# Performance work log

Hardware: AMD Instinct MI355X
Metric: run time of the kernel (lower is better)

## Reference

```python
import jax, jax.numpy as jnp
import numpy as np

N_NODES = 50000
N_REL = 8
N_EDGES = 100000
IN_SIZE = 128
OUT_SIZE = 128


def setup_inputs() -> dict:
    key = jax.random.key(0)
    k1, k2, k3, k4, k5 = jax.random.split(key, 5)
    inp = jax.random.normal(k1, (N_NODES, IN_SIZE), dtype=jnp.float32)
    src = jax.random.randint(k2, (N_REL, N_EDGES), 0, N_NODES, dtype=jnp.int32)
    dst = jax.random.randint(k3, (N_REL, N_EDGES), 0, N_NODES, dtype=jnp.int32)
    vals = jax.random.uniform(k4, (N_REL, N_EDGES), dtype=jnp.float32)
    weights = jax.random.normal(k5, (N_REL, IN_SIZE, OUT_SIZE), dtype=jnp.float32) * (1.0 / np.sqrt(IN_SIZE))
    return {"inp": inp, "src": src, "dst": dst, "vals": vals, "weights": weights}


def reference(inp, src, dst, vals, weights):
    # Per-relation sparse adj @ inp:  agg[r] = A_r @ inp, A_r given as COO edges.
    n_nodes = inp.shape[0]

    def rel_agg(s, d, v):
        msgs = v[:, None] * inp[s]                      # [E, in]
        return jax.ops.segment_sum(msgs, d, num_segments=n_nodes)  # [N, in]

    agg = jax.vmap(rel_agg)(src, dst, vals)             # [R, N, in]
    # concat along features then block-stacked weight matmul == per-relation
    # matmul summed over relations: out = sum_r agg[r] @ W[r]
    out = jnp.einsum('rni,rio->no', agg, weights)       # [N, out]
    return out
```

## Files before the change

### kernel.cpp

```cpp
#include <hip/hip_runtime.h>


constexpr int IN  = 128;
constexpr int OUT = 128;
constexpr int LDK = 136;
constexpr int NPB = 64;
constexpr int NGRP = 512;
constexpr int MAXE = 2048;
constexpr int NXCD = 8;
constexpr int CPAD = 16;

typedef __attribute__((ext_vector_type(8))) short bf16x8;
typedef __attribute__((ext_vector_type(4))) float f32x4;

__device__ inline unsigned short f2bf(float f) {
    unsigned int u = __float_as_uint(f);
    u += 0x7fffu + ((u >> 16) & 1u);
    return (unsigned short)(u >> 16);
}
__device__ inline float bflo(unsigned int u) { return __uint_as_float(u << 16); }
__device__ inline float bfhi(unsigned int u) { return __uint_as_float(u & 0xffff0000u); }

__global__ __launch_bounds__(256) void conv_inp_kernel(
    const float* __restrict__ x, unsigned short* __restrict__ y, int n8)
{
    const int i = blockIdx.x * 256 + threadIdx.x;
    if (i >= n8) return;
    const float4 a = ((const float4*)x)[i * 2];
    const float4 b = ((const float4*)x)[i * 2 + 1];
    uint4 o;
    o.x = (unsigned)f2bf(a.x) | ((unsigned)f2bf(a.y) << 16);
    o.y = (unsigned)f2bf(a.z) | ((unsigned)f2bf(a.w) << 16);
    o.z = (unsigned)f2bf(b.x) | ((unsigned)f2bf(b.y) << 16);
    o.w = (unsigned)f2bf(b.z) | ((unsigned)f2bf(b.w) << 16);
    ((uint4*)y)[i] = o;
}

__global__ __launch_bounds__(256) void conv_w_kernel(
    const float* __restrict__ w, unsigned short* __restrict__ wt, int total)
{
    const int t = blockIdx.x * 256 + threadIdx.x;
    if (t >= total) return;
    const int r = t >> 14, rem = t & 16383;
    const int n = rem >> 7, k = rem & 127;
    wt[t] = f2bf(w[(r << 14) + (k << 7) + n]);
}

__global__ __launch_bounds__(256) void prep_kernel(
    const float* __restrict__ x, unsigned short* __restrict__ y, int n8, int nbI,
    const float* __restrict__ w, unsigned short* __restrict__ wtb, int wtot, int nbW,
    const int* __restrict__ src, const int* __restrict__ dst,
    const float* __restrict__ vals, int* __restrict__ bin_cnt,
    int2* __restrict__ binned, int4* __restrict__ spill,
    int* __restrict__ spill_cnt,
    int n_edges, int n_nodes, int nbins, int cap, int spill_max, int fill_gx)
{
    const int bid = blockIdx.x;
    const int tid = threadIdx.x;
    if (bid < nbI) {
        const int i = bid * 256 + tid;
        if (i >= n8) return;
        const float4 a = ((const float4*)x)[i * 2];
        const float4 b = ((const float4*)x)[i * 2 + 1];
        uint4 o;
        o.x = (unsigned)f2bf(a.x) | ((unsigned)f2bf(a.y) << 16);
        o.y = (unsigned)f2bf(a.z) | ((unsigned)f2bf(a.w) << 16);
        o.z = (unsigned)f2bf(b.x) | ((unsigned)f2bf(b.y) << 16);
        o.w = (unsigned)f2bf(b.z) | ((unsigned)f2bf(b.w) << 16);
        ((uint4*)y)[i] = o;
        return;
    }
    if (bid < nbI + nbW) {
        const int t = (bid - nbI) * 256 + tid;
        if (t >= wtot) return;
        const int r = t >> 14, rem = t & 16383;
        const int n = rem >> 7, k = rem & 127;
        wtb[t] = f2bf(w[(r << 14) + (k << 7) + n]);
        return;
    }
    int xcd;
    asm volatile("s_getreg_b32 %0, hwreg(HW_REG_XCC_ID)" : "=s"(xcd));
    xcd &= (NXCD - 1);
    const int idx = bid - nbI - nbW;
    const int rel = idx / fill_gx;
    const int e = (idx - rel * fill_gx) * 256 + tid;
    if (e >= n_edges) return;
    const size_t g = (size_t)rel * n_edges + e;
    const int d = dst[g];
    const int s = src[g];
    const int bin = d >> 6;
    const int packed = (rel << 25) | ((d & 63) << 19) | s;
    const int cell = xcd * nbins + bin;
    const int pos = atomicAdd(&bin_cnt[cell * CPAD], 1);
    if (pos < cap) {
        binned[(size_t)cell * cap + pos] =
            make_int2(packed, __float_as_int(vals[g]));
    } else {
        const int sp = atomicAdd(spill_cnt, 1);
        if (sp < spill_max)
            spill[sp] = make_int4(d, (rel << 19) | s, __float_as_int(vals[g]), 0);
    }
}

__global__ __launch_bounds__(256) void bin_gather_gemm(
    const unsigned short* __restrict__ inpb,
    const unsigned short* __restrict__ wt,
    const int2* __restrict__ binned, const int* __restrict__ bin_cnt,
    float* __restrict__ out, int n_nodes, int nbins, int cap, int n_rel)
{
    __shared__ int2 sorted[MAXE];
    __shared__ unsigned short A[64 * LDK];
    __shared__ int lcnt[NGRP], loff[NGRP], lcur[NGRP];
    __shared__ int cellcnt[NXCD];

    const int bin = blockIdx.x;
    const int tid = threadIdx.x;

    for (int i = tid; i < NGRP; i += 256) lcnt[i] = 0;
    if (tid < NXCD) {
        int c = bin_cnt[(tid * nbins + bin) * CPAD];
        cellcnt[tid] = c > cap ? cap : c;
    }
    __syncthreads();

    for (int xc = 0; xc < NXCD; ++xc) {
        const int cnt = cellcnt[xc];
        const int2* __restrict__ b = binned + (size_t)(xc * nbins + bin) * cap;
        for (int i = tid; i < cnt; i += 256)
            atomicAdd(&lcnt[(b[i].x >> 19) & (NGRP - 1)], 1);
    }
    __syncthreads();

    if (tid < 64) {
        const int base = tid * 8;
        int v[8]; int s = 0;
        #pragma unroll
        for (int i = 0; i < 8; ++i) { v[i] = s; s += lcnt[base + i]; }
        int incl = s;
        #pragma unroll
        for (int off = 1; off < 64; off <<= 1) {
            int t = __shfl_up(incl, off, 64);
            if (tid >= off) incl += t;
        }
        const int excl = incl - s;
        #pragma unroll
        for (int i = 0; i < 8; ++i) loff[base + i] = excl + v[i];
    }
    for (int i = tid; i < NGRP; i += 256) lcur[i] = 0;
    __syncthreads();

    for (int xc = 0; xc < NXCD; ++xc) {
        const int cnt = cellcnt[xc];
        const int2* __restrict__ b = binned + (size_t)(xc * nbins + bin) * cap;
        for (int i = tid; i < cnt; i += 256) {
            const int2 e = b[i];
            const int g = (e.x >> 19) & (NGRP - 1);
            const int pos = atomicAdd(&lcur[g], 1);
            sorted[loff[g] + pos] = e;
        }
    }
    __syncthreads();

    const int wave = tid >> 6, lane = tid & 63;
    const int m = lane & 15, q = lane >> 4;
    const int hw = tid >> 5, hlane = tid & 31;

    f32x4 acc[4][2];
    #pragma unroll
    for (int mt = 0; mt < 4; ++mt) {
        acc[mt][0] = (f32x4){0.f, 0.f, 0.f, 0.f};
        acc[mt][1] = (f32x4){0.f, 0.f, 0.f, 0.f};
    }

    for (int r = 0; r < n_rel; ++r) {
        #pragma unroll
        for (int k = 0; k < 8; ++k) {
            const int ln = hw * 8 + k;
            const int g = r * 64 + ln;
            const int base = loff[g], cnt = lcnt[g];
            float4 a4 = make_float4(0.f, 0.f, 0.f, 0.f);
            int j = 0;
            for (; j + 4 <= cnt; j += 4) {
                const int2 r0 = sorted[base + j],     r1 = sorted[base + j + 1];
                const int2 r2 = sorted[base + j + 2], r3 = sorted[base + j + 3];
                const uint2 h0 = ((const uint2*)(inpb + (size_t)(r0.x & 0x7ffff) * IN))[hlane];
                const uint2 h1 = ((const uint2*)(inpb + (size_t)(r1.x & 0x7ffff) * IN))[hlane];
                const uint2 h2 = ((const uint2*)(inpb + (size_t)(r2.x & 0x7ffff) * IN))[hlane];
                const uint2 h3 = ((const uint2*)(inpb + (size_t)(r3.x & 0x7ffff) * IN))[hlane];
                const float v0 = __int_as_float(r0.y), v1 = __int_as_float(r1.y);
                const float v2 = __int_as_float(r2.y), v3 = __int_as_float(r3.y);
                a4.x += v0*bflo(h0.x) + v1*bflo(h1.x) + v2*bflo(h2.x) + v3*bflo(h3.x);
                a4.y += v0*bfhi(h0.x) + v1*bfhi(h1.x) + v2*bfhi(h2.x) + v3*bfhi(h3.x);
                a4.z += v0*bflo(h0.y) + v1*bflo(h1.y) + v2*bflo(h2.y) + v3*bflo(h3.y);
                a4.w += v0*bfhi(h0.y) + v1*bfhi(h1.y) + v2*bfhi(h2.y) + v3*bfhi(h3.y);
            }
            for (; j < cnt; ++j) {
                const int2 r0 = sorted[base + j];
                const float v = __int_as_float(r0.y);
                const uint2 hv = ((const uint2*)(inpb + (size_t)(r0.x & 0x7ffff) * IN))[hlane];
                a4.x += v * bflo(hv.x); a4.y += v * bfhi(hv.x);
                a4.z += v * bflo(hv.y); a4.w += v * bfhi(hv.y);
            }
            uint2 o;
            o.x = (unsigned)f2bf(a4.x) | ((unsigned)f2bf(a4.y) << 16);
            o.y = (unsigned)f2bf(a4.z) | ((unsigned)f2bf(a4.w) << 16);
            *(uint2*)&A[ln * LDK + hlane * 4] = o;
        }
        __syncthreads();

        const unsigned short* wtr = wt + ((size_t)r * OUT + wave * 32) * IN;
        bf16x8 bfrag[2][4];
        #pragma unroll
        for (int nt = 0; nt < 2; ++nt)
            #pragma unroll
            for (int ks = 0; ks < 4; ++ks)
                bfrag[nt][ks] = *(const bf16x8*)(
                    wtr + (size_t)(nt * 16 + m) * IN + ks * 32 + q * 8);

        #pragma unroll
        for (int ks = 0; ks < 4; ++ks) {
            bf16x8 a[4];
            #pragma unroll
            for (int mt = 0; mt < 4; ++mt)
                a[mt] = *(const bf16x8*)&A[(mt * 16 + m) * LDK + ks * 32 + q * 8];
            #pragma unroll
            for (int mt = 0; mt < 4; ++mt) {
                acc[mt][0] = __builtin_amdgcn_mfma_f32_16x16x32_bf16(
                    a[mt], bfrag[0][ks], acc[mt][0], 0, 0, 0);
                acc[mt][1] = __builtin_amdgcn_mfma_f32_16x16x32_bf16(
                    a[mt], bfrag[1][ks], acc[mt][1], 0, 0, 0);
            }
        }
        __syncthreads();
    }

    const int row0 = bin * NPB;
    #pragma unroll
    for (int mt = 0; mt < 4; ++mt) {
        #pragma unroll
        for (int rg = 0; rg < 4; ++rg) {
            const int row = row0 + mt * 16 + q * 4 + rg;
            if (row < n_nodes) {
                float* op = out + (size_t)row * OUT + wave * 32 + m;
                op[0]  = acc[mt][0][rg];
                op[16] = acc[mt][1][rg];
            }
        }
    }
}

__global__ __launch_bounds__(256) void spill_w_kernel(
    const unsigned short* __restrict__ inpb,
    const unsigned short* __restrict__ wt,
    const int4* __restrict__ spill, const int* __restrict__ spill_cnt,
    float* __restrict__ out, int spill_max)
{
    int n = *spill_cnt;
    if (n > spill_max) n = spill_max;
    const int w = (blockIdx.x * 256 + threadIdx.x) >> 6;
    const int lane = threadIdx.x & 63;
    const int nw = gridDim.x * 4;
    for (int i = w; i < n; i += nw) {
        const int4 s = spill[i];
        const int d = s.x;
        const int rel = s.y >> 19, srcrow = s.y & 0x7ffff;
        const float v = __int_as_float(s.z);
        const unsigned short* irow = inpb + (size_t)srcrow * IN;
        #pragma unroll
        for (int cc = 0; cc < 2; ++cc) {
            const int col = lane * 2 + cc;
            const unsigned short* wrow = wt + ((size_t)rel * OUT + col) * IN;
            float acc = 0.f;
            for (int k8 = 0; k8 < IN; k8 += 8) {
                const uint4 iw = *(const uint4*)(irow + k8);
                const uint4 ww = *(const uint4*)(wrow + k8);
                acc += bflo(iw.x)*bflo(ww.x) + bfhi(iw.x)*bfhi(ww.x)
                     + bflo(iw.y)*bflo(ww.y) + bfhi(iw.y)*bfhi(ww.y)
                     + bflo(iw.z)*bflo(ww.z) + bfhi(iw.z)*bfhi(ww.z)
                     + bflo(iw.w)*bflo(ww.w) + bfhi(iw.w)*bfhi(ww.w);
            }
            __hip_atomic_fetch_add(out + (size_t)d * OUT + col, v * acc,
                                   __ATOMIC_RELAXED, __HIP_MEMORY_SCOPE_AGENT);
        }
    }
}

__global__ __launch_bounds__(256) void mfma_gemm(
    const unsigned short* __restrict__ inpb,
    const unsigned short* __restrict__ wt,
    unsigned short* __restrict__ h, int rel_base, int n_nodes)
{
    __shared__ unsigned short As[128 * LDK];

    const int rel = rel_base + blockIdx.y;
    const int row0 = blockIdx.x * 128;
    const int tid = threadIdx.x;
    const int wave = tid >> 6, lane = tid & 63;
    const int m = lane & 15, q = lane >> 4;

    {
        const int r = tid >> 1;
        const int half = (tid & 1) * 64;
        const int grow = row0 + r;
        const uint4* gp = (const uint4*)(inpb + (size_t)grow * IN + half);
        uint4* lp = (uint4*)&As[r * LDK + half];
        #pragma unroll
        for (int i = 0; i < 8; ++i) {
            uint4 v = make_uint4(0u, 0u, 0u, 0u);
            if (grow < n_nodes) v = gp[i];
            lp[i] = v;
        }
    }

    bf16x8 bfrag[2][4];
    {
        const unsigned short* wtr = wt + ((size_t)rel * OUT + wave * 32) * IN;
        #pragma unroll
        for (int nt = 0; nt < 2; ++nt)
            #pragma unroll
            for (int ks = 0; ks < 4; ++ks)
                bfrag[nt][ks] = *(const bf16x8*)(
                    wtr + (size_t)(nt * 16 + m) * IN + ks * 32 + q * 8);
    }

    __syncthreads();

    f32x4 acc[8][2];
    #pragma unroll
    for (int mt = 0; mt < 8; ++mt)
        #pragma unroll
        for (int nt = 0; nt < 2; ++nt)
            acc[mt][nt] = (f32x4){0.f, 0.f, 0.f, 0.f};

    #pragma unroll
    for (int ks = 0; ks < 4; ++ks) {
        bf16x8 a[8];
        #pragma unroll
        for (int mt = 0; mt < 8; ++mt)
            a[mt] = *(const bf16x8*)&As[(mt * 16 + m) * LDK + ks * 32 + q * 8];
        #pragma unroll
        for (int mt = 0; mt < 8; ++mt) {
            acc[mt][0] = __builtin_amdgcn_mfma_f32_16x16x32_bf16(
                a[mt], bfrag[0][ks], acc[mt][0], 0, 0, 0);
            acc[mt][1] = __builtin_amdgcn_mfma_f32_16x16x32_bf16(
                a[mt], bfrag[1][ks], acc[mt][1], 0, 0, 0);
        }
    }

    unsigned short* hrel = h + (size_t)blockIdx.y * n_nodes * OUT;
    #pragma unroll
    for (int mt = 0; mt < 8; ++mt) {
        #pragma unroll
        for (int rg = 0; rg < 4; ++rg) {
            const int row = row0 + mt * 16 + q * 4 + rg;
            if (row < n_nodes) {
                unsigned short* hp = hrel + (size_t)row * OUT + wave * 32 + m;
                hp[0]  = f2bf(acc[mt][0][rg]);
                hp[16] = f2bf(acc[mt][1][rg]);
            }
        }
    }
}

__global__ __launch_bounds__(256) void fill_kernel(
    const int* __restrict__ src, const int* __restrict__ dst,
    const float* __restrict__ vals, int* __restrict__ counts,
    int2* __restrict__ bucket, int4* __restrict__ spill,
    int* __restrict__ spill_cnt, int n_edges, int n_nodes,
    int cap, int spill_max)
{
    const int e = blockIdx.x * 256 + threadIdx.x;
    if (e >= n_edges) return;
    const size_t g = (size_t)blockIdx.y * n_edges + e;
    const int d = dst[g];
    const int enc = blockIdx.y * n_nodes + src[g];
    const int pos = atomicAdd(&counts[d], 1);
    if (pos < cap) {
        bucket[(size_t)d * cap + pos] = make_int2(enc, __float_as_int(vals[g]));
    } else {
        const int sp = atomicAdd(spill_cnt, 1);
        if (sp < spill_max)
            spill[sp] = make_int4(d, enc, __float_as_int(vals[g]), 0);
    }
}

__global__ __launch_bounds__(256) void gather_kernel(
    const unsigned short* __restrict__ h, const int2* __restrict__ bucket,
    const int* __restrict__ counts, float* __restrict__ out,
    int n_nodes, int cap, int accum)
{
    const int node = blockIdx.x * 8 + (threadIdx.x >> 5);
    const int lane = threadIdx.x & 31;
    if (node >= n_nodes) return;
    int cnt = counts[node];
    if (cnt > cap) cnt = cap;
    const int2* __restrict__ b = bucket + (size_t)node * cap;
    float4* __restrict__ op = (float4*)(out + (size_t)node * OUT);

    float4 acc = accum ? op[lane] : make_float4(0.f, 0.f, 0.f, 0.f);
    int j = 0;
    for (; j + 4 <= cnt; j += 4) {
        const int2 r0 = b[j], r1 = b[j + 1], r2 = b[j + 2], r3 = b[j + 3];
        const uint2 h0 = ((const uint2*)(h + (size_t)r0.x * OUT))[lane];
        const uint2 h1 = ((const uint2*)(h + (size_t)r1.x * OUT))[lane];
        const uint2 h2 = ((const uint2*)(h + (size_t)r2.x * OUT))[lane];
        const uint2 h3 = ((const uint2*)(h + (size_t)r3.x * OUT))[lane];
        const float v0 = __int_as_float(r0.y), v1 = __int_as_float(r1.y);
        const float v2 = __int_as_float(r2.y), v3 = __int_as_float(r3.y);
        acc.x += v0*bflo(h0.x) + v1*bflo(h1.x) + v2*bflo(h2.x) + v3*bflo(h3.x);
        acc.y += v0*bfhi(h0.x) + v1*bfhi(h1.x) + v2*bfhi(h2.x) + v3*bfhi(h3.x);
        acc.z += v0*bflo(h0.y) + v1*bflo(h1.y) + v2*bflo(h2.y) + v3*bflo(h3.y);
        acc.w += v0*bfhi(h0.y) + v1*bfhi(h1.y) + v2*bfhi(h2.y) + v3*bfhi(h3.y);
    }
    for (; j < cnt; ++j) {
        const int2 r0 = b[j];
        const float v = __int_as_float(r0.y);
        const uint2 hv = ((const uint2*)(h + (size_t)r0.x * OUT))[lane];
        acc.x += v * bflo(hv.x); acc.y += v * bfhi(hv.x);
        acc.z += v * bflo(hv.y); acc.w += v * bfhi(hv.y);
    }
    op[lane] = acc;
}

__global__ __launch_bounds__(256) void spill_kernel(
    const unsigned short* __restrict__ h, const int4* __restrict__ spill,
    const int* __restrict__ spill_cnt, float* __restrict__ out, int spill_max)
{
    int n = *spill_cnt;
    if (n > spill_max) n = spill_max;
    const int w = (blockIdx.x * 256 + threadIdx.x) >> 6;
    const int lane = threadIdx.x & 63;
    const int nw = gridDim.x * 4;
    for (int i = w; i < n; i += nw) {
        const int4 s = spill[i];
        const float v = __int_as_float(s.z);
        const unsigned int u = ((const unsigned int*)(h + (size_t)s.y * OUT))[lane];
        float* __restrict__ orow = out + (size_t)s.x * OUT;
        __hip_atomic_fetch_add(orow + lane * 2,     v * bflo(u),
                               __ATOMIC_RELAXED, __HIP_MEMORY_SCOPE_AGENT);
        __hip_atomic_fetch_add(orow + lane * 2 + 1, v * bfhi(u),
                               __ATOMIC_RELAXED, __HIP_MEMORY_SCOPE_AGENT);
    }
}

__global__ __launch_bounds__(256) void scatter_kernel(
    const unsigned short* __restrict__ h, const int* __restrict__ src,
    const int* __restrict__ dst, const float* __restrict__ vals,
    float* __restrict__ out, int n_edges)
{
    const int e = blockIdx.x * 8 + (threadIdx.x >> 5);
    if (e >= n_edges) return;
    const int lane = threadIdx.x & 31;
    const int s = src[e];
    const int d = dst[e];
    const float v = vals[e];
    const unsigned int* __restrict__ hrow =
        (const unsigned int*)(h + (size_t)s * OUT);
    float* __restrict__ orow = out + (size_t)d * OUT;
    #pragma unroll
    for (int kk = 0; kk < 2; ++kk) {
        const int jj = lane + kk * 32;
        const unsigned int u = hrow[jj];
        __hip_atomic_fetch_add(orow + jj * 2,     v * bflo(u),
                               __ATOMIC_RELAXED, __HIP_MEMORY_SCOPE_AGENT);
        __hip_atomic_fetch_add(orow + jj * 2 + 1, v * bfhi(u),
                               __ATOMIC_RELAXED, __HIP_MEMORY_SCOPE_AGENT);
    }
}

extern "C" void kernel_launch(void* const* d_in, const int* in_sizes, int n_in,
                              void* d_out, int out_size, void* d_ws, size_t ws_size,
                              hipStream_t stream) {
    const float* inp     = (const float*)d_in[0];
    const int*   src     = (const int*)  d_in[1];
    const int*   dst     = (const int*)  d_in[2];
    const float* vals    = (const float*)d_in[3];
    const float* weights = (const float*)d_in[4];
    float* out = (float*)d_out;

    const int n_nodes = in_sizes[0] / IN;
    const int n_rel   = in_sizes[4] / (IN * OUT);
    const int n_edges = in_sizes[1] / n_rel;

    auto align_up = [](size_t x) { return (x + 255) & ~(size_t)255; };
    const int SPILL_MAX = 65536;
    const size_t sz_inpb   = align_up((size_t)n_nodes * IN * 2);
    const size_t sz_wt     = align_up((size_t)n_rel * IN * OUT * 2);
    const size_t sz_spill  = align_up((size_t)SPILL_MAX * 16);

    const int conv_n8 = n_nodes * IN / 8;
    const int wt_tot  = n_rel * IN * OUT;
    const int gemm_gx = (n_nodes + 127) / 128;
    const int gath_gx = (n_nodes + 7) / 8;
    const int fill_gx = (n_edges + 255) / 256;
    const int nbins   = (n_nodes + NPB - 1) / NPB;

    if (n_rel <= 8 && n_nodes < (1 << 19)) {
        const size_t sz_bcnt = align_up(((size_t)NXCD * nbins * CPAD + CPAD) * 4);
        int cap = 0;
        const int caps[] = {256, 192};
        for (int c : caps) {
            const size_t sz_binned = align_up((size_t)NXCD * nbins * c * 8);
            if (sz_inpb + sz_wt + sz_bcnt + sz_spill + sz_binned <= ws_size) {
                cap = c; break;
            }
        }
        if (cap > 0) {
            const size_t sz_binned = align_up((size_t)NXCD * nbins * cap * 8);
            char* p = (char*)d_ws;
            unsigned short* inpb = (unsigned short*)p;  p += sz_inpb;
            unsigned short* wtb  = (unsigned short*)p;  p += sz_wt;
            int*   bin_cnt = (int*)p;   p += sz_bcnt;
            int4*  spill   = (int4*)p;  p += sz_spill;
            int2*  binned  = (int2*)p;  p += sz_binned;
            int*   spill_cnt = bin_cnt + (size_t)NXCD * nbins * CPAD;

            const int nbI = (conv_n8 + 255) / 256;
            const int nbW = (wt_tot + 255) / 256;
            const int nF  = fill_gx * n_rel;

            hipMemsetAsync(bin_cnt, 0,
                           ((size_t)NXCD * nbins * CPAD + CPAD) * 4, stream);
            prep_kernel<<<nbI + nbW + nF, 256, 0, stream>>>(
                inp, inpb, conv_n8, nbI, weights, wtb, wt_tot, nbW,
                src, dst, vals, bin_cnt, binned, spill, spill_cnt,
                n_edges, n_nodes, nbins, cap, SPILL_MAX, fill_gx);
            bin_gather_gemm<<<nbins, 256, 0, stream>>>(
                inpb, wtb, binned, bin_cnt, out, n_nodes, nbins, cap, n_rel);
            spill_w_kernel<<<128, 256, 0, stream>>>(
                inpb, wtb, spill, spill_cnt, out, SPILL_MAX);
            return;
        }
    }

    const size_t sz_counts = align_up((size_t)(n_nodes + 1) * 4);
    const size_t fixed = sz_inpb + sz_wt + sz_counts + sz_spill;

    {
        const size_t sz_h = (size_t)n_rel * n_nodes * OUT * 2;
        int cap = 0;
        const int caps[] = {64, 48, 32, 24, 20};
        for (int c : caps) {
            if (fixed + sz_h + align_up((size_t)n_nodes * c * 8) <= ws_size) {
                cap = c; break;
            }
        }
        if (cap > 0) {
            char* p = (char*)d_ws;
            unsigned short* inpb = (unsigned short*)p;  p += sz_inpb;
            unsigned short* wtb  = (unsigned short*)p;  p += sz_wt;
            int*   counts = (int*)p;    p += sz_counts;
            int4*  spill  = (int4*)p;   p += sz_spill;
            unsigned short* h = (unsigned short*)p;     p += sz_h;
            int2*  bucket = (int2*)p;
            int*   spill_cnt = counts + n_nodes;

            conv_inp_kernel<<<(conv_n8 + 255) / 256, 256, 0, stream>>>(
                inp, inpb, conv_n8);
            conv_w_kernel<<<(wt_tot + 255) / 256, 256, 0, stream>>>(
                weights, wtb, wt_tot);
            hipMemsetAsync(counts, 0, (size_t)(n_nodes + 1) * 4, stream);
            dim3 fg(fill_gx, n_rel);
            fill_kernel<<<fg, 256, 0, stream>>>(src, dst, vals, counts, bucket,
                                                spill, spill_cnt, n_edges,
                                                n_nodes, cap, SPILL_MAX);
            dim3 gg(gemm_gx, n_rel);
            mfma_gemm<<<gg, 256, 0, stream>>>(inpb, wtb, h, 0, n_nodes);
            gather_kernel<<<gath_gx, 256, 0, stream>>>(h, bucket, counts, out,
                                                       n_nodes, cap, 0);
            spill_kernel<<<128, 256, 0, stream>>>(h, spill, spill_cnt, out,
                                                  SPILL_MAX);
            return;
        }
    }

    {
        char* p = (char*)d_ws;
        unsigned short* inpb = (unsigned short*)p;  p += sz_inpb;
        unsigned short* wtb  = (unsigned short*)p;  p += sz_wt;
        unsigned short* h = (unsigned short*)p;

        conv_inp_kernel<<<(conv_n8 + 255) / 256, 256, 0, stream>>>(
            inp, inpb, conv_n8);
        conv_w_kernel<<<(wt_tot + 255) / 256, 256, 0, stream>>>(
            weights, wtb, wt_tot);
        hipMemsetAsync(out, 0, (size_t)n_nodes * OUT * 4, stream);
        const int sgx = (n_edges + 7) / 8;
        for (int r = 0; r < n_rel; ++r) {
            const size_t eoff = (size_t)r * n_edges;
            dim3 gg(gemm_gx, 1);
            mfma_gemm<<<gg, 256, 0, stream>>>(inpb, wtb, h, r, n_nodes);
            scatter_kernel<<<sgx, 256, 0, stream>>>(h, src + eoff, dst + eoff,
                                                    vals + eoff, out, n_edges);
        }
    }
}
```

Before: 221.6 us.

## Bin edges per relation and aggregate via LDS float atomics instead of sorting

Edge binning cells now include the relation index, so each block reads per-relation lists directly and drops the in-block counting sort over 512 groups. Aggregation switches from a per-row serial gather to parallel edge processing that scatters into an fp32 LDS tile with atomicAdd, then converts to bf16 when loading MFMA fragments. This removes the sort passes and evens out load imbalance across destination rows, but adds many LDS atomics, a larger fp32 tile, and more bin-count cells to memset and read.

```diff
diff --git a/kernel.cpp b/kernel.cpp
--- a/kernel.cpp
+++ b/kernel.cpp
@@ -5,8 +5,8 @@
 constexpr int OUT = 128;
 constexpr int LDK = 136;
 constexpr int NPB = 64;
-constexpr int NGRP = 512;
-constexpr int MAXE = 2048;
+constexpr int LDA = 132;
+constexpr int MAXT = 512;
 constexpr int NXCD = 8;
 constexpr int CPAD = 16;
 
@@ -20,6 +20,9 @@
 }
 __device__ inline float bflo(unsigned int u) { return __uint_as_float(u << 16); }
 __device__ inline float bfhi(unsigned int u) { return __uint_as_float(u & 0xffff0000u); }
+__device__ inline unsigned int pack2bf(float a, float b) {
+    return (unsigned)f2bf(a) | ((unsigned)f2bf(b) << 16);
+}
 
 __global__ __launch_bounds__(256) void conv_inp_kernel(
     const float* __restrict__ x, unsigned short* __restrict__ y, int n8)
@@ -29,10 +32,10 @@
     const float4 a = ((const float4*)x)[i * 2];
     const float4 b = ((const float4*)x)[i * 2 + 1];
     uint4 o;
-    o.x = (unsigned)f2bf(a.x) | ((unsigned)f2bf(a.y) << 16);
-    o.y = (unsigned)f2bf(a.z) | ((unsigned)f2bf(a.w) << 16);
-    o.z = (unsigned)f2bf(b.x) | ((unsigned)f2bf(b.y) << 16);
-    o.w = (unsigned)f2bf(b.z) | ((unsigned)f2bf(b.w) << 16);
+    o.x = pack2bf(a.x, a.y);
+    o.y = pack2bf(a.z, a.w);
+    o.z = pack2bf(b.x, b.y);
+    o.w = pack2bf(b.z, b.w);
     ((uint4*)y)[i] = o;
 }
 
@@ -53,7 +56,8 @@
     const float* __restrict__ vals, int* __restrict__ bin_cnt,
     int2* __restrict__ binned, int4* __restrict__ spill,
     int* __restrict__ spill_cnt,
-    int n_edges, int n_nodes, int nbins, int cap, int spill_max, int fill_gx)
+    int n_edges, int n_nodes, int nbins, int cap, int spill_max,
+    int fill_gx, int n_rel)
 {
     const int bid = blockIdx.x;
     const int tid = threadIdx.x;
@@ -63,10 +67,10 @@
         const float4 a = ((const float4*)x)[i * 2];
         const float4 b = ((const float4*)x)[i * 2 + 1];
         uint4 o;
-        o.x = (unsigned)f2bf(a.x) | ((unsigned)f2bf(a.y) << 16);
-        o.y = (unsigned)f2bf(a.z) | ((unsigned)f2bf(a.w) << 16);
-        o.z = (unsigned)f2bf(b.x) | ((unsigned)f2bf(b.y) << 16);
-        o.w = (unsigned)f2bf(b.z) | ((unsigned)f2bf(b.w) << 16);
+        o.x = pack2bf(a.x, a.y);
+        o.y = pack2bf(a.z, a.w);
+        o.z = pack2bf(b.x, b.y);
+        o.w = pack2bf(b.z, b.w);
         ((uint4*)y)[i] = o;
         return;
     }
@@ -89,8 +93,8 @@
     const int d = dst[g];
     const int s = src[g];
     const int bin = d >> 6;
-    const int packed = (rel << 25) | ((d & 63) << 19) | s;
-    const int cell = xcd * nbins + bin;
+    const int packed = ((d & 63) << 19) | s;
+    const int cell = (xcd * n_rel + rel) * nbins + bin;
     const int pos = atomicAdd(&bin_cnt[cell * CPAD], 1);
     if (pos < cap) {
         binned[(size_t)cell * cap + pos] =
@@ -102,68 +106,39 @@
     }
 }
 
-__global__ __launch_bounds__(256) void bin_gather_gemm(
+__global__ __launch_bounds__(256, 4) void bin_gemm_kernel(
     const unsigned short* __restrict__ inpb,
     const unsigned short* __restrict__ wt,
     const int2* __restrict__ binned, const int* __restrict__ bin_cnt,
     float* __restrict__ out, int n_nodes, int nbins, int cap, int n_rel)
 {
-    __shared__ int2 sorted[MAXE];
-    __shared__ unsigned short A[64 * LDK];
-    __shared__ int lcnt[NGRP], loff[NGRP], lcur[NGRP];
-    __shared__ int cellcnt[NXCD];
+    __shared__ float A[NPB * LDA];
+    __shared__ int2 ent[MAXT];
+    __shared__ int cnt_lds[NXCD * 8];
+    __shared__ int coff[8][NXCD + 1];
 
     const int bin = blockIdx.x;
     const int tid = threadIdx.x;
 
-    for (int i = tid; i < NGRP; i += 256) lcnt[i] = 0;
-    if (tid < NXCD) {
-        int c = bin_cnt[(tid * nbins + bin) * CPAD];
-        cellcnt[tid] = c > cap ? cap : c;
+    if (tid < NXCD * n_rel) {
+        const int x = tid / n_rel, r = tid - x * n_rel;
+        int c = bin_cnt[((x * n_rel + r) * nbins + bin) * CPAD];
+        cnt_lds[x * n_rel + r] = c > cap ? cap : c;
     }
     __syncthreads();
-
-    for (int xc = 0; xc < NXCD; ++xc) {
-        const int cnt = cellcnt[xc];
-        const int2* __restrict__ b = binned + (size_t)(xc * nbins + bin) * cap;
-        for (int i = tid; i < cnt; i += 256)
-            atomicAdd(&lcnt[(b[i].x >> 19) & (NGRP - 1)], 1);
-    }
-    __syncthreads();
-
-    if (tid < 64) {
-        const int base = tid * 8;
-        int v[8]; int s = 0;
-        #pragma unroll
-        for (int i = 0; i < 8; ++i) { v[i] = s; s += lcnt[base + i]; }
-        int incl = s;
-        #pragma unroll
-        for (int off = 1; off < 64; off <<= 1) {
-            int t = __shfl_up(incl, off, 64);
-            if (tid >= off) incl += t;
-        }
-        const int excl = incl - s;
-        #pragma unroll
-        for (int i = 0; i < 8; ++i) loff[base + i] = excl + v[i];
-    }
-    for (int i = tid; i < NGRP; i += 256) lcur[i] = 0;
-    __syncthreads();
-
-    for (int xc = 0; xc < NXCD; ++xc) {
-        const int cnt = cellcnt[xc];
-        const int2* __restrict__ b = binned + (size_t)(xc * nbins + bin) * cap;
-        for (int i = tid; i < cnt; i += 256) {
-            const int2 e = b[i];
-            const int g = (e.x >> 19) & (NGRP - 1);
-            const int pos = atomicAdd(&lcur[g], 1);
-            sorted[loff[g] + pos] = e;
-        }
-    }
-    __syncthreads();
+    if (tid < n_rel) {
+        int s = 0;
+        coff[tid][0] = 0;
+        #pragma unroll
+        for (int x = 0; x < NXCD; ++x) {
+            s += cnt_lds[x * n_rel + tid];
+            coff[tid][x + 1] = s;
+        }
+    }
 
     const int wave = tid >> 6, lane = tid & 63;
     const int m = lane & 15, q = lane >> 4;
-    const int hw = tid >> 5, hlane = tid & 31;
+    const int qtr = (tid >> 4) & 3, l16 = tid & 15;
 
     f32x4 acc[4][2];
     #pragma unroll
@@ -173,38 +148,49 @@
     }
 
     for (int r = 0; r < n_rel; ++r) {
-        #pragma unroll
-        for (int k = 0; k < 8; ++k) {
-            const int ln = hw * 8 + k;
-            const int g = r * 64 + ln;
-            const int base = loff[g], cnt = lcnt[g];
-            float4 a4 = make_float4(0.f, 0.f, 0.f, 0.f);
-            int j = 0;
-            for (; j + 4 <= cnt; j += 4) {
-                const int2 r0 = sorted[base + j],     r1 = sorted[base + j + 1];
-                const int2 r2 = sorted[base + j + 2], r3 = sorted[base + j + 3];
-                const uint2 h0 = ((const uint2*)(inpb + (size_t)(r0.x & 0x7ffff) * IN))[hlane];
-                const uint2 h1 = ((const uint2*)(inpb + (size_t)(r1.x & 0x7ffff) * IN))[hlane];
-                const uint2 h2 = ((const uint2*)(inpb + (size_t)(r2.x & 0x7ffff) * IN))[hlane];
-                const uint2 h3 = ((const uint2*)(inpb + (size_t)(r3.x & 0x7ffff) * IN))[hlane];
-                const float v0 = __int_as_float(r0.y), v1 = __int_as_float(r1.y);
-                const float v2 = __int_as_float(r2.y), v3 = __int_as_float(r3.y);
-                a4.x += v0*bflo(h0.x) + v1*bflo(h1.x) + v2*bflo(h2.x) + v3*bflo(h3.x);
-                a4.y += v0*bfhi(h0.x) + v1*bfhi(h1.x) + v2*bfhi(h2.x) + v3*bfhi(h3.x);
-                a4.z += v0*bflo(h0.y) + v1*bflo(h1.y) + v2*bflo(h2.y) + v3*bflo(h3.y);
-                a4.w += v0*bfhi(h0.y) + v1*bfhi(h1.y) + v2*bfhi(h2.y) + v3*bfhi(h3.y);
-            }
-            for (; j < cnt; ++j) {
-                const int2 r0 = sorted[base + j];
-                const float v = __int_as_float(r0.y);
-                const uint2 hv = ((const uint2*)(inpb + (size_t)(r0.x & 0x7ffff) * IN))[hlane];
-                a4.x += v * bflo(hv.x); a4.y += v * bfhi(hv.x);
-                a4.z += v * bflo(hv.y); a4.w += v * bfhi(hv.y);
-            }
-            uint2 o;
-            o.x = (unsigned)f2bf(a4.x) | ((unsigned)f2bf(a4.y) << 16);
-            o.y = (unsigned)f2bf(a4.z) | ((unsigned)f2bf(a4.w) << 16);
-            *(uint2*)&A[ln * LDK + hlane * 4] = o;
+        __syncthreads();
+
+        {
+            float* zp = &A[(tid >> 2) * LDA + (tid & 3) * 32];
+            #pragma unroll
+            for (int i = 0; i < 8; ++i)
+                *(float4*)(zp + i * 4) = make_float4(0.f, 0.f, 0.f, 0.f);
+        }
+        const int T = coff[r][NXCD];
+        for (int i = tid; i < T; i += 256) {
+            int xc = 0;
+            #pragma unroll
+            for (int j = 1; j < NXCD; ++j) xc += (i >= coff[r][j]);
+            const int pos = i - coff[r][xc];
+            ent[i] = binned[(size_t)((xc * n_rel + r) * nbins + bin) * cap + pos];
+        }
+        __syncthreads();
+
+        for (int base = wave * 16 + qtr * 4; base < T; base += 64) {
+            int2 e[4];
+            #pragma unroll
+            for (int k = 0; k < 4; ++k) {
+                const int idx = base + k;
+                e[k] = (idx < T) ? ent[idx] : make_int2(0, 0);
+            }
+            uint4 rw[4];
+            #pragma unroll
+            for (int k = 0; k < 4; ++k)
+                rw[k] = ((const uint4*)(inpb +
+                         (size_t)(e[k].x & 0x7ffff) * IN))[l16];
+            #pragma unroll
+            for (int k = 0; k < 4; ++k) {
+                const float v = __int_as_float(e[k].y);
+                float* Ar = &A[((e[k].x >> 19) & 63) * LDA + l16 * 8];
+                atomicAdd(Ar + 0, v * bflo(rw[k].x));
+                atomicAdd(Ar + 1, v * bfhi(rw[k].x));
+                atomicAdd(Ar + 2, v * bflo(rw[k].y));
+                atomicAdd(Ar + 3, v * bfhi(rw[k].y));
+                atomicAdd(Ar + 4, v * bflo(rw[k].z));
+                atomicAdd(Ar + 5, v * bfhi(rw[k].z));
+                atomicAdd(Ar + 6, v * bflo(rw[k].w));
+                atomicAdd(Ar + 7, v * bfhi(rw[k].w));
+            }
         }
         __syncthreads();
 
@@ -221,8 +207,15 @@
         for (int ks = 0; ks < 4; ++ks) {
             bf16x8 a[4];
             #pragma unroll
-            for (int mt = 0; mt < 4; ++mt)
-                a[mt] = *(const bf16x8*)&A[(mt * 16 + m) * LDK + ks * 32 + q * 8];
+            for (int mt = 0; mt < 4; ++mt) {
+                const float* Ap = &A[(mt * 16 + m) * LDA + ks * 32 + q * 8];
+                const float4 lo = *(const float4*)Ap;
+                const float4 hi = *(const float4*)(Ap + 4);
+                union { uint4 u; bf16x8 v; } cv;
+                cv.u = make_uint4(pack2bf(lo.x, lo.y), pack2bf(lo.z, lo.w),
+                                  pack2bf(hi.x, hi.y), pack2bf(hi.z, hi.w));
+                a[mt] = cv.v;
+            }
             #pragma unroll
             for (int mt = 0; mt < 4; ++mt) {
                 acc[mt][0] = __builtin_amdgcn_mfma_f32_16x16x32_bf16(
@@ -231,7 +224,6 @@
                     a[mt], bfrag[1][ks], acc[mt][1], 0, 0, 0);
             }
         }
-        __syncthreads();
     }
 
     const int row0 = bin * NPB;
@@ -496,36 +488,36 @@
     const int nbins   = (n_nodes + NPB - 1) / NPB;
 
     if (n_rel <= 8 && n_nodes < (1 << 19)) {
-        const size_t sz_bcnt = align_up(((size_t)NXCD * nbins * CPAD + CPAD) * 4);
+        const size_t ncells  = (size_t)NXCD * n_rel * nbins;
+        const size_t sz_bcnt = align_up((ncells * CPAD + CPAD) * 4);
         int cap = 0;
-        const int caps[] = {256, 192};
+        const int caps[] = {64, 48, 32};
         for (int c : caps) {
-            const size_t sz_binned = align_up((size_t)NXCD * nbins * c * 8);
+            const size_t sz_binned = align_up(ncells * c * 8);
             if (sz_inpb + sz_wt + sz_bcnt + sz_spill + sz_binned <= ws_size) {
                 cap = c; break;
             }
         }
         if (cap > 0) {
-            const size_t sz_binned = align_up((size_t)NXCD * nbins * cap * 8);
+            const size_t sz_binned = align_up(ncells * cap * 8);
             char* p = (char*)d_ws;
             unsigned short* inpb = (unsigned short*)p;  p += sz_inpb;
             unsigned short* wtb  = (unsigned short*)p;  p += sz_wt;
             int*   bin_cnt = (int*)p;   p += sz_bcnt;
             int4*  spill   = (int4*)p;  p += sz_spill;
             int2*  binned  = (int2*)p;  p += sz_binned;
-            int*   spill_cnt = bin_cnt + (size_t)NXCD * nbins * CPAD;
+            int*   spill_cnt = bin_cnt + ncells * CPAD;
 
             const int nbI = (conv_n8 + 255) / 256;
             const int nbW = (wt_tot + 255) / 256;
             const int nF  = fill_gx * n_rel;
 
-            hipMemsetAsync(bin_cnt, 0,
-                           ((size_t)NXCD * nbins * CPAD + CPAD) * 4, stream);
+            hipMemsetAsync(bin_cnt, 0, (ncells * CPAD + CPAD) * 4, stream);
             prep_kernel<<<nbI + nbW + nF, 256, 0, stream>>>(
                 inp, inpb, conv_n8, nbI, weights, wtb, wt_tot, nbW,
                 src, dst, vals, bin_cnt, binned, spill, spill_cnt,
-                n_edges, n_nodes, nbins, cap, SPILL_MAX, fill_gx);
-            bin_gather_gemm<<<nbins, 256, 0, stream>>>(
+                n_edges, n_nodes, nbins, cap, SPILL_MAX, fill_gx, n_rel);
+            bin_gemm_kernel<<<nbins, 256, 0, stream>>>(
                 inpb, wtb, binned, bin_cnt, out, n_nodes, nbins, cap, n_rel);
             spill_w_kernel<<<128, 256, 0, stream>>>(
                 inpb, wtb, spill, spill_cnt, out, SPILL_MAX);
```

Result: slower. 853.4 us (+285.1%).
